# Optimization experiments

Hardware: AMD Instinct MI355X
Metric: run time of the kernel (lower is better)

The kernel has to match this reference:

```python
import jax, jax.numpy as jnp
import numpy as np

EPS = 1e-5


def setup_inputs() -> dict:
    key = jax.random.key(0)
    k1, k2, k3 = jax.random.split(key, 3)
    B, C, H, W = 32, 512, 56, 56
    R = 16
    x = jax.random.normal(k1, (B, C, H, W), dtype=jnp.float32)
    # SE excitation weights (no bias): Linear(C -> C//R), Linear(C//R -> C)
    w1 = jax.random.normal(k2, (C // R, C), dtype=jnp.float32) * (1.0 / np.sqrt(C))
    w2 = jax.random.normal(k3, (C, C // R), dtype=jnp.float32) * (1.0 / np.sqrt(C // R))
    # BatchNorm2d affine params (init: weight=1, bias=0)
    bn_weight = jnp.ones((C,), dtype=jnp.float32)
    bn_bias = jnp.zeros((C,), dtype=jnp.float32)
    return {"x": x, "w1": w1, "w2": w2, "bn_weight": bn_weight, "bn_bias": bn_bias}


def reference(x, w1, w2, bn_weight, bn_bias):
    B, C, H, W = x.shape
    # squeeze: global average pool -> [B, C]
    s = jnp.mean(x, axis=(2, 3))
    # excitation: Linear -> ReLU -> Linear -> Sigmoid
    e = jax.nn.sigmoid(jax.nn.relu(s @ w1.T) @ w2.T)  # [B, C]
    # scale
    y = x * e[:, :, None, None]  # [B, C, H, W]
    # BatchNorm2d (training-mode batch statistics, biased variance)
    mean = jnp.mean(y, axis=(0, 2, 3))
    var = jnp.var(y, axis=(0, 2, 3))
    yn = (y - mean[None, :, None, None]) * (
        bn_weight[None, :, None, None] * jax.lax.rsqrt(var + EPS)[None, :, None, None]
    ) + bn_bias[None, :, None, None]
    # unsqueeze dim=1 (c1=1) then rearrange 'b c1 (c2 c3) h w -> b c2 (c1 c3) h w', c2=2
    z = yn.reshape(B, 2, C // 2, H, W)
    # flatten(-2).mean(-1): mean over spatial dims -> [B, 2, C//2]
    z = jnp.mean(z, axis=(3, 4))
    # sum over dim=1 -> [B, C//2]
    return jnp.sum(z, axis=1)
```

## Files before the change

### kernel.cpp

```cpp
#include <hip/hip_runtime.h>
#include <math.h>

constexpr int B  = 32;
constexpr int C  = 512;
constexpr int CR = 32;
constexpr int HW = 56 * 56;
constexpr int NV4 = HW / 4;
constexpr float EPS = 1e-5f;

__global__ __launch_bounds__(256) void rowstats(const float* __restrict__ x,
                                                float* __restrict__ s_out,
                                                float* __restrict__ q_out) {
    const int wid  = threadIdx.x >> 6;
    const int lane = threadIdx.x & 63;
    const int row  = blockIdx.x * 4 + wid;
    const float4* xp = reinterpret_cast<const float4*>(x) + (size_t)row * NV4 + lane;
    float s = 0.f, q = 0.f;
    #pragma unroll
    for (int i = 0; i < 12; ++i) {
        float4 v = xp[i * 64];
        s += (v.x + v.y) + (v.z + v.w);
        q += (v.x * v.x + v.y * v.y) + (v.z * v.z + v.w * v.w);
    }
    if (lane < 16) {
        float4 v = xp[768];
        s += (v.x + v.y) + (v.z + v.w);
        q += (v.x * v.x + v.y * v.y) + (v.z * v.z + v.w * v.w);
    }
    #pragma unroll
    for (int off = 32; off > 0; off >>= 1) {
        s += __shfl_down(s, off, 64);
        q += __shfl_down(q, off, 64);
    }
    if (lane == 0) {
        s_out[row] = s * (1.0f / (float)HW);
        q_out[row] = q;
    }
}

__global__ __launch_bounds__(512) void excite(const float* __restrict__ s_in,
                                              const float* __restrict__ q_in,
                                              const float* __restrict__ w1,
                                              const float* __restrict__ w2,
                                              float* __restrict__ m_out,
                                              float* __restrict__ eq_out) {
    const int b   = blockIdx.x;
    const int tid = threadIdx.x;
    __shared__ __align__(16) float sh_s[C];
    __shared__ float sh_h[CR];

    sh_s[tid] = s_in[b * C + tid];
    __syncthreads();

    {
        const int j = tid >> 4, t = tid & 15;
        const float4* wr = reinterpret_cast<const float4*>(w1 + j * C);
        const float4* sr = reinterpret_cast<const float4*>(sh_s);
        float acc = 0.f;
        #pragma unroll
        for (int k = 0; k < 8; ++k) {
            float4 wv = wr[t + 16 * k];
            float4 sv = sr[t + 16 * k];
            acc = fmaf(sv.x, wv.x, fmaf(sv.y, wv.y, fmaf(sv.z, wv.z, fmaf(sv.w, wv.w, acc))));
        }
        #pragma unroll
        for (int off = 8; off > 0; off >>= 1)
            acc += __shfl_down(acc, off, 16);
        if (t == 0) sh_h[j] = fmaxf(acc, 0.f);
    }
    __syncthreads();

    {
        const int c = tid;
        const float4* w2p = reinterpret_cast<const float4*>(w2 + c * CR);
        const float4* hp  = reinterpret_cast<const float4*>(sh_h);
        float acc = 0.f;
        #pragma unroll
        for (int k = 0; k < CR / 4; ++k) {
            float4 wv = w2p[k];
            float4 hv = hp[k];
            acc = fmaf(hv.x, wv.x, fmaf(hv.y, wv.y, fmaf(hv.z, wv.z, fmaf(hv.w, wv.w, acc))));
        }
        const float e = 1.0f / (1.0f + expf(-acc));
        m_out[b * C + c]  = e * sh_s[c];
        eq_out[b * C + c] = e * e * q_in[b * C + c];
    }
}

__global__ __launch_bounds__(512) void bnout(const float* __restrict__ m_in,
                                             const float* __restrict__ eq_in,
                                             const float* __restrict__ bnw,
                                             const float* __restrict__ bnb,
                                             float* __restrict__ out) {
    const int c = threadIdx.x;
    __shared__ float sh_z[B][C / 2];
    float mv[B];
    float mean = 0.f, eq = 0.f;
    #pragma unroll
    for (int b = 0; b < B; ++b) {
        mv[b] = m_in[b * C + c];
        mean += mv[b];
        eq   += eq_in[b * C + c];
    }
    mean *= (1.0f / (float)B);
    const float var = eq * (1.0f / ((float)B * (float)HW)) - mean * mean;
    const float g   = bnw[c] * rsqrtf(var + EPS);
    const float bb  = bnb[c];

    if (c < C / 2) {
        #pragma unroll
        for (int b = 0; b < B; ++b)
            sh_z[b][c] = (mv[b] - mean) * g + bb;
    }
    __syncthreads();
    if (c >= C / 2) {
        const int c2 = c - C / 2;
        #pragma unroll
        for (int b = 0; b < B; ++b)
            out[b * (C / 2) + c2] = sh_z[b][c2] + ((mv[b] - mean) * g + bb);
    }
}

extern "C" void kernel_launch(void* const* d_in, const int* in_sizes, int n_in,
                              void* d_out, int out_size, void* d_ws, size_t ws_size,
                              hipStream_t stream) {
    const float* x   = (const float*)d_in[0];
    const float* w1  = (const float*)d_in[1];
    const float* w2  = (const float*)d_in[2];
    const float* bnw = (const float*)d_in[3];
    const float* bnb = (const float*)d_in[4];
    float* out = (float*)d_out;

    float* s_ws  = (float*)d_ws;
    float* q_ws  = s_ws + B * C;
    float* m_ws  = q_ws + B * C;
    float* eq_ws = m_ws + B * C;

    rowstats<<<dim3(B * C / 4), dim3(256), 0, stream>>>(x, s_ws, q_ws);
    excite<<<dim3(B), dim3(512), 0, stream>>>(s_ws, q_ws, w1, w2, m_ws, eq_ws);
    bnout<<<dim3(1), dim3(512), 0, stream>>>(m_ws, eq_ws, bnw, bnb, out);
}
```

Baseline: 42.60 us.

## Fuse excite and BN-output kernels via last-block atomic ticket

Merges the excitation kernel and the single-block batch-norm output kernel into one launch. Each block takes a ticket from an atomic counter, and the last block to finish computes the BN statistics and the output; the counter is reset inside the rowstats kernel. The intent is to save one kernel launch and its inter-kernel gap. The cost is an extra threadfence and atomic per block, plus a larger shared-memory footprint in every block. The tail of each row is also changed from a masked float4 load by 16 lanes to a scalar load by all 64 lanes.

```diff
diff --git a/kernel.cpp b/kernel.cpp
--- a/kernel.cpp
+++ b/kernel.cpp
@@ -10,7 +10,9 @@
 
 __global__ __launch_bounds__(256) void rowstats(const float* __restrict__ x,
                                                 float* __restrict__ s_out,
-                                                float* __restrict__ q_out) {
+                                                float* __restrict__ q_out,
+                                                unsigned int* __restrict__ counter) {
+    if (blockIdx.x == 0 && threadIdx.x == 0) *counter = 0u;
     const int wid  = threadIdx.x >> 6;
     const int lane = threadIdx.x & 63;
     const int row  = blockIdx.x * 4 + wid;
@@ -22,10 +24,10 @@
         s += (v.x + v.y) + (v.z + v.w);
         q += (v.x * v.x + v.y * v.y) + (v.z * v.z + v.w * v.w);
     }
-    if (lane < 16) {
-        float4 v = xp[768];
-        s += (v.x + v.y) + (v.z + v.w);
-        q += (v.x * v.x + v.y * v.y) + (v.z * v.z + v.w * v.w);
+    {
+        const float v = x[(size_t)row * HW + 3072 + lane];
+        s += v;
+        q = fmaf(v, v, q);
     }
     #pragma unroll
     for (int off = 32; off > 0; off >>= 1) {
@@ -38,16 +40,22 @@
     }
 }
 
-__global__ __launch_bounds__(512) void excite(const float* __restrict__ s_in,
-                                              const float* __restrict__ q_in,
-                                              const float* __restrict__ w1,
-                                              const float* __restrict__ w2,
-                                              float* __restrict__ m_out,
-                                              float* __restrict__ eq_out) {
+__global__ __launch_bounds__(512) void excite_bn(const float* __restrict__ s_in,
+                                                 const float* __restrict__ q_in,
+                                                 const float* __restrict__ w1,
+                                                 const float* __restrict__ w2,
+                                                 const float* __restrict__ bnw,
+                                                 const float* __restrict__ bnb,
+                                                 float* __restrict__ m_ws,
+                                                 float* __restrict__ eq_ws,
+                                                 unsigned int* __restrict__ counter,
+                                                 float* __restrict__ out) {
     const int b   = blockIdx.x;
     const int tid = threadIdx.x;
     __shared__ __align__(16) float sh_s[C];
     __shared__ float sh_h[CR];
+    __shared__ unsigned int sh_ticket;
+    __shared__ float sh_z[B][C / 2];
 
     sh_s[tid] = s_in[b * C + tid];
     __syncthreads();
@@ -71,8 +79,7 @@
     __syncthreads();
 
     {
-        const int c = tid;
-        const float4* w2p = reinterpret_cast<const float4*>(w2 + c * CR);
+        const float4* w2p = reinterpret_cast<const float4*>(w2 + tid * CR);
         const float4* hp  = reinterpret_cast<const float4*>(sh_h);
         float acc = 0.f;
         #pragma unroll
@@ -82,42 +89,44 @@
             acc = fmaf(hv.x, wv.x, fmaf(hv.y, wv.y, fmaf(hv.z, wv.z, fmaf(hv.w, wv.w, acc))));
         }
         const float e = 1.0f / (1.0f + expf(-acc));
-        m_out[b * C + c]  = e * sh_s[c];
-        eq_out[b * C + c] = e * e * q_in[b * C + c];
+        m_ws[b * C + tid]  = e * sh_s[tid];
+        eq_ws[b * C + tid] = e * e * q_in[b * C + tid];
     }
-}
 
-__global__ __launch_bounds__(512) void bnout(const float* __restrict__ m_in,
-                                             const float* __restrict__ eq_in,
-                                             const float* __restrict__ bnw,
-                                             const float* __restrict__ bnb,
-                                             float* __restrict__ out) {
-    const int c = threadIdx.x;
-    __shared__ float sh_z[B][C / 2];
-    float mv[B];
-    float mean = 0.f, eq = 0.f;
-    #pragma unroll
-    for (int b = 0; b < B; ++b) {
-        mv[b] = m_in[b * C + c];
-        mean += mv[b];
-        eq   += eq_in[b * C + c];
-    }
-    mean *= (1.0f / (float)B);
-    const float var = eq * (1.0f / ((float)B * (float)HW)) - mean * mean;
-    const float g   = bnw[c] * rsqrtf(var + EPS);
-    const float bb  = bnb[c];
+    __threadfence();
+    __syncthreads();
+    if (tid == 0) sh_ticket = atomicAdd(counter, 1u);
+    __syncthreads();
+    if (sh_ticket != (unsigned int)(B - 1)) return;
+    __threadfence();
 
-    if (c < C / 2) {
+    {
+        const int c = tid;
+        float mv[B];
+        float mean = 0.f, eq = 0.f;
         #pragma unroll
-        for (int b = 0; b < B; ++b)
-            sh_z[b][c] = (mv[b] - mean) * g + bb;
-    }
-    __syncthreads();
-    if (c >= C / 2) {
-        const int c2 = c - C / 2;
-        #pragma unroll
-        for (int b = 0; b < B; ++b)
-            out[b * (C / 2) + c2] = sh_z[b][c2] + ((mv[b] - mean) * g + bb);
+        for (int bb = 0; bb < B; ++bb) {
+            mv[bb] = m_ws[bb * C + c];
+            mean += mv[bb];
+            eq   += eq_ws[bb * C + c];
+        }
+        mean *= (1.0f / (float)B);
+        const float var = eq * (1.0f / ((float)B * (float)HW)) - mean * mean;
+        const float g   = bnw[c] * rsqrtf(var + EPS);
+        const float bia = bnb[c];
+
+        if (c < C / 2) {
+            #pragma unroll
+            for (int bb = 0; bb < B; ++bb)
+                sh_z[bb][c] = (mv[bb] - mean) * g + bia;
+        }
+        __syncthreads();
+        if (c >= C / 2) {
+            const int c2 = c - C / 2;
+            #pragma unroll
+            for (int bb = 0; bb < B; ++bb)
+                out[bb * (C / 2) + c2] = sh_z[bb][c2] + ((mv[bb] - mean) * g + bia);
+        }
     }
 }
 
@@ -135,8 +144,9 @@
     float* q_ws  = s_ws + B * C;
     float* m_ws  = q_ws + B * C;
     float* eq_ws = m_ws + B * C;
+    unsigned int* counter = (unsigned int*)(eq_ws + B * C);
 
-    rowstats<<<dim3(B * C / 4), dim3(256), 0, stream>>>(x, s_ws, q_ws);
-    excite<<<dim3(B), dim3(512), 0, stream>>>(s_ws, q_ws, w1, w2, m_ws, eq_ws);
-    bnout<<<dim3(1), dim3(512), 0, stream>>>(m_ws, eq_ws, bnw, bnb, out);
+    rowstats<<<dim3(B * C / 4), dim3(256), 0, stream>>>(x, s_ws, q_ws, counter);
+    excite_bn<<<dim3(B), dim3(512), 0, stream>>>(s_ws, q_ws, w1, w2, bnw, bnb,
+                                                 m_ws, eq_ws, counter, out);
 }
```

Result: slower. 46.44 us (+9.0%).
